# Kernel tuning notes

Measured on AMD Instinct MI355X. Metric: run time of the kernel, lower is better.

The kernel has to match this reference:

```python
import jax, jax.numpy as jnp
import numpy as np

B, C, N = 8, 128, 2048
HEADS = 4
OUT = 128
HD = OUT // HEADS  # 32


def setup_inputs() -> dict:
    key = jax.random.key(0)
    kx, kq, kk, kv, ko = jax.random.split(key, 5)
    # xavier_uniform bounds
    def xavier(k, shape, fan_in, fan_out):
        a = float(np.sqrt(6.0 / (fan_in + fan_out)))
        return jax.random.uniform(k, shape, jnp.float32, -a, a)
    return {
        "x": jax.random.normal(kx, (B, C, N), jnp.float32),
        "W_q": xavier(kq, (HEADS, C, HD), C, HD),
        "W_k": xavier(kk, (HEADS, C, HD), C, HD),
        "W_v": xavier(kv, (HEADS, C, HD), C, HD),
        "W_o": xavier(ko, (OUT, OUT), OUT, OUT),
    }


def reference(x, W_q, W_k, W_v, W_o):
    # x: [B, C, N] -> x_t: [B, N, C]
    x_t = jnp.transpose(x, (0, 2, 1))
    # per-head projections: [B, H, N, d]
    q = jnp.einsum("bnc,hcd->bhnd", x_t, W_q)
    k = jnp.einsum("bnc,hcd->bhnd", x_t, W_k)
    v = jnp.einsum("bnc,hcd->bhnd", x_t, W_v)
    scale = 1.0 / jnp.sqrt(jnp.asarray(HD, jnp.float32))
    # materialized score matrix [B, H, N, N]
    scores = jax.nn.softmax(jnp.einsum("bhnd,bhmd->bhnm", q, k) * scale, axis=-1)
    # weighted sum per head then concat heads: [B, N, H*d]
    out = jnp.einsum("bhnm,bhmd->bhnd", scores, v)
    out = jnp.transpose(out, (0, 2, 1, 3)).reshape(B, N, OUT)
    out = out @ W_o  # [B, N, OUT]
    adj = jnp.mean(scores, axis=1)  # [B, N, N]
    return jnp.transpose(out, (0, 2, 1)), adj
```

## Files before the change

kernel.cpp:

```cpp
#include <hip/hip_runtime.h>
#include <hip/hip_bf16.h>

#define NB 8
#define NC 128
#define NN 2048
#define NH 4
#define HD 32
#define NOUT 128
#define QB 16

typedef _Float16 half8 __attribute__((ext_vector_type(8)));
typedef _Float16 half4 __attribute__((ext_vector_type(4)));
typedef float f32x4 __attribute__((ext_vector_type(4)));

__device__ __forceinline__ f32x4 mfma16(half8 a, half8 b, f32x4 c) {
  return __builtin_amdgcn_mfma_f32_16x16x32_f16(a, b, c, 0, 0, 0);
}

__global__ __launch_bounds__(256) void k_prep(
    const float* __restrict__ Wq, const float* __restrict__ Wk,
    const float* __restrict__ Wv, const float* __restrict__ Wo,
    _Float16* __restrict__ WqT, _Float16* __restrict__ WkT,
    _Float16* __restrict__ WvT, _Float16* __restrict__ WoT)
{
  int id = blockIdx.x * 256 + threadIdx.x;
  if (id < 3 * 16384) {
    int m = id >> 14, rem = id & 16383;
    int h = rem >> 12, d = (rem >> 7) & 31, c = rem & 127;
    const float* W = (m == 0) ? Wq : (m == 1) ? Wk : Wv;
    _Float16* WT   = (m == 0) ? WqT : (m == 1) ? WkT : WvT;
    WT[(h * 32 + d) * 128 + c] = (_Float16)W[(h * 128 + c) * 32 + d];
  } else {
    int j = id - 49152;
    int o = j >> 7, c = j & 127;
    WoT[o * 128 + c] = (_Float16)Wo[c * 128 + o];
  }
}

__global__ __launch_bounds__(256) void k_proj(
    const float* __restrict__ x, const _Float16* __restrict__ WqT,
    const _Float16* __restrict__ WkT, const _Float16* __restrict__ WvT,
    _Float16* __restrict__ qo, _Float16* __restrict__ ko, _Float16* __restrict__ vto)
{
  __shared__ _Float16 xs[32][136];
  const int bid = blockIdx.x;
  const int b  = bid & 7;
  const int n0 = (bid >> 3) * 32;
  const int tid = threadIdx.x;
  const int h = tid >> 6, l = tid & 63, lr = l & 15, lg = l >> 4;

  {
    int c  = tid >> 1;
    int nq = (tid & 1) * 16;
    const float* src = x + (size_t)(b * NC + c) * NN + n0 + nq;
#pragma unroll
    for (int i = 0; i < 4; ++i) {
      f32x4 v = *(const f32x4*)(src + i * 4);
#pragma unroll
      for (int j = 0; j < 4; ++j) xs[nq + i * 4 + j][c] = (_Float16)v[j];
    }
  }
  __syncthreads();

  half8 a[2][4];
#pragma unroll
  for (int rf = 0; rf < 2; ++rf)
#pragma unroll
    for (int kc = 0; kc < 4; ++kc)
      a[rf][kc] = *(const half8*)(&xs[rf * 16 + lr][kc * 32 + lg * 8]);

#pragma unroll
  for (int m = 0; m < 2; ++m) {
    const _Float16* WT = m ? WkT : WqT;
    _Float16* dst      = m ? ko : qo;
    f32x4 acc[2][2] = {};
#pragma unroll
    for (int kc = 0; kc < 4; ++kc) {
      half8 wb[2];
#pragma unroll
      for (int cf = 0; cf < 2; ++cf)
        wb[cf] = *(const half8*)(WT + (size_t)(h * HD + cf * 16 + lr) * NC + kc * 32 + lg * 8);
#pragma unroll
      for (int rf = 0; rf < 2; ++rf)
#pragma unroll
        for (int cf = 0; cf < 2; ++cf)
          acc[rf][cf] = mfma16(a[rf][kc], wb[cf], acc[rf][cf]);
    }
#pragma unroll
    for (int rf = 0; rf < 2; ++rf)
#pragma unroll
      for (int cf = 0; cf < 2; ++cf)
#pragma unroll
        for (int r = 0; r < 4; ++r)
          dst[((size_t)(b * NH + h) * NN + n0 + rf * 16 + lg * 4 + r) * HD + cf * 16 + lr] =
              (_Float16)acc[rf][cf][r];
  }

  {
    f32x4 acc[2][2] = {};
#pragma unroll
    for (int kc = 0; kc < 4; ++kc) {
      half8 aw[2];
#pragma unroll
      for (int rf = 0; rf < 2; ++rf)
        aw[rf] = *(const half8*)(WvT + (size_t)(h * HD + rf * 16 + lr) * NC + kc * 32 + lg * 8);
#pragma unroll
      for (int rf = 0; rf < 2; ++rf)
#pragma unroll
        for (int nf = 0; nf < 2; ++nf)
          acc[rf][nf] = mfma16(aw[rf], a[nf][kc], acc[rf][nf]);
    }
#pragma unroll
    for (int rf = 0; rf < 2; ++rf)
#pragma unroll
      for (int nf = 0; nf < 2; ++nf)
#pragma unroll
        for (int r = 0; r < 4; ++r)
          vto[((size_t)(b * NH + h) * HD + rf * 16 + lg * 4 + r) * NN + n0 + nf * 16 + lr] =
              (_Float16)acc[rf][nf][r];
  }
}

union SMem {
  _Float16 p[NH * QB * 72];
  struct { _Float16 ocat[QB * 136]; float ot[128 * 20]; } ep;
};

__global__ __launch_bounds__(256) void k_attn(
    const _Float16* __restrict__ q, const _Float16* __restrict__ k,
    const _Float16* __restrict__ vt, const _Float16* __restrict__ WoT,
    float* __restrict__ outT, float* __restrict__ adj)
{
  __shared__ SMem sm;
  const int bid = blockIdx.x;
  const int b  = bid & 7;
  const int n0 = (bid >> 3) * QB;
  const int h  = threadIdx.x >> 6;
  const int l  = threadIdx.x & 63;
  const int lr = l & 15, lg = l >> 4;

  const _Float16* qh = q  + (size_t)(b * NH + h) * NN * HD;
  const _Float16* kh = k  + (size_t)(b * NH + h) * NN * HD;
  const _Float16* vh = vt + (size_t)(b * NH + h) * HD * NN;

  half8 qa = *(const half8*)(qh + (size_t)(n0 + lr) * HD + lg * 8);

  const float c1 = 0.25504527f;
  const float c2 = 17.3123405f;

  float rs[4] = {};
  for (int mt = 0; mt < NN / 32; ++mt) {
    half8 kb0 = *(const half8*)(kh + (size_t)(mt * 32 + lr) * HD + lg * 8);
    half8 kb1 = *(const half8*)(kh + (size_t)(mt * 32 + 16 + lr) * HD + lg * 8);
    f32x4 z{};
    f32x4 s0 = mfma16(qa, kb0, z);
    f32x4 s1 = mfma16(qa, kb1, z);
#pragma unroll
    for (int r = 0; r < 4; ++r)
      rs[r] += __builtin_amdgcn_exp2f(s0[r] * c1 - c2) +
               __builtin_amdgcn_exp2f(s1[r] * c1 - c2);
  }
#pragma unroll
  for (int r = 0; r < 4; ++r) {
    float v = rs[r];
    v += __shfl_xor(v, 1); v += __shfl_xor(v, 2);
    v += __shfl_xor(v, 4); v += __shfl_xor(v, 8);
    rs[r] = 1.0f / v;
  }

  f32x4 oacc[2] = {};
  const int tr = threadIdx.x >> 4;
  const int tc = (threadIdx.x & 15) * 4;

  for (int mt2 = 0; mt2 < NN / 64; ++mt2) {
#pragma unroll
    for (int st = 0; st < 4; ++st) {
      half8 kb = *(const half8*)(kh + (size_t)(mt2 * 64 + st * 16 + lr) * HD + lg * 8);
      f32x4 z{};
      f32x4 s = mfma16(qa, kb, z);
#pragma unroll
      for (int r = 0; r < 4; ++r)
        sm.p[(h * QB + lg * 4 + r) * 72 + st * 16 + lr] =
            (_Float16)(__builtin_amdgcn_exp2f(s[r] * c1 - c2) * rs[r]);
    }
    __syncthreads();
#pragma unroll
    for (int kc = 0; kc < 2; ++kc) {
      half8 pa  = *(const half8*)(&sm.p[(h * QB + lr) * 72 + kc * 32 + lg * 8]);
      half8 vb0 = *(const half8*)(vh + (size_t)lr * NN        + mt2 * 64 + kc * 32 + lg * 8);
      half8 vb1 = *(const half8*)(vh + (size_t)(16 + lr) * NN + mt2 * 64 + kc * 32 + lg * 8);
      oacc[0] = mfma16(pa, vb0, oacc[0]);
      oacc[1] = mfma16(pa, vb1, oacc[1]);
    }
    {
      float a4[4] = {};
#pragma unroll
      for (int h2 = 0; h2 < 4; ++h2) {
        half4 pv = *(const half4*)(&sm.p[(h2 * QB + tr) * 72 + tc]);
#pragma unroll
        for (int i = 0; i < 4; ++i) a4[i] += (float)pv[i];
      }
      f32x4 w = {a4[0] * 0.25f, a4[1] * 0.25f, a4[2] * 0.25f, a4[3] * 0.25f};
      *(f32x4*)(adj + ((size_t)(b * NN) + n0 + tr) * NN + mt2 * 64 + tc) = w;
    }
    __syncthreads();
  }

#pragma unroll
  for (int df = 0; df < 2; ++df)
#pragma unroll
    for (int r = 0; r < 4; ++r)
      sm.ep.ocat[(lg * 4 + r) * 136 + h * 32 + df * 16 + lr] = (_Float16)oacc[df][r];
  __syncthreads();

  f32x4 o2[2] = {};
#pragma unroll
  for (int kc = 0; kc < 4; ++kc) {
    half8 a2 = *(const half8*)(&sm.ep.ocat[lr * 136 + kc * 32 + lg * 8]);
#pragma unroll
    for (int of = 0; of < 2; ++of) {
      half8 wb = *(const half8*)(WoT + (size_t)(h * 32 + of * 16 + lr) * NOUT + kc * 32 + lg * 8);
      o2[of] = mfma16(a2, wb, o2[of]);
    }
  }
#pragma unroll
  for (int of = 0; of < 2; ++of)
#pragma unroll
    for (int r = 0; r < 4; ++r)
      sm.ep.ot[(h * 32 + of * 16 + lr) * 20 + lg * 4 + r] = o2[of][r];
  __syncthreads();
  {
    int o  = threadIdx.x >> 1;
    int hf = threadIdx.x & 1;
    float* dst = outT + ((size_t)(b * NOUT) + o) * NN + n0 + hf * 8;
    *(f32x4*)(dst)     = *(const f32x4*)(&sm.ep.ot[o * 20 + hf * 8]);
    *(f32x4*)(dst + 4) = *(const f32x4*)(&sm.ep.ot[o * 20 + hf * 8 + 4]);
  }
}

extern "C" void kernel_launch(void* const* d_in, const int* in_sizes, int n_in,
                              void* d_out, int out_size, void* d_ws, size_t ws_size,
                              hipStream_t stream) {
  const float* x  = (const float*)d_in[0];
  const float* Wq = (const float*)d_in[1];
  const float* Wk = (const float*)d_in[2];
  const float* Wv = (const float*)d_in[3];
  const float* Wo = (const float*)d_in[4];

  float* outT = (float*)d_out;
  float* adj  = outT + (size_t)NB * NOUT * NN;

  const size_t qkv_elems = (size_t)NB * NH * NN * HD;
  _Float16* qw  = (_Float16*)d_ws;
  _Float16* kw  = qw + qkv_elems;
  _Float16* vw  = kw + qkv_elems;
  _Float16* wqT = vw + qkv_elems;
  _Float16* wkT = wqT + 16384;
  _Float16* wvT = wkT + 16384;
  _Float16* woT = wvT + 16384;

  k_prep<<<dim3(256), dim3(256), 0, stream>>>(Wq, Wk, Wv, Wo, wqT, wkT, wvT, woT);
  k_proj<<<dim3(NB * (NN / 32)), dim3(256), 0, stream>>>(x, wqT, wkT, wvT, qw, kw, vw);
  k_attn<<<dim3(NB * (NN / QB)), dim3(256), 0, stream>>>(qw, kw, vw, woT, outT, adj);
}
```

Baseline: 267.1 us.

## Split key dimension across waves with all heads per wave, keep P in registers

```diff
diff --git a/kernel.cpp b/kernel.cpp
--- a/kernel.cpp
+++ b/kernel.cpp
@@ -15,6 +15,9 @@
 
 __device__ __forceinline__ f32x4 mfma16(half8 a, half8 b, f32x4 c) {
   return __builtin_amdgcn_mfma_f32_16x16x32_f16(a, b, c, 0, 0, 0);
+}
+__device__ __forceinline__ f32x4 mfma16k16(half4 a, half4 b, f32x4 c) {
+  return __builtin_amdgcn_mfma_f32_16x16x16f16(a, b, c, 0, 0, 0);
 }
 
 __global__ __launch_bounds__(256) void k_prep(
@@ -121,120 +124,169 @@
   }
 }
 
-union SMem {
-  _Float16 p[NH * QB * 72];
-  struct { _Float16 ocat[QB * 136]; float ot[128 * 20]; } ep;
-};
-
-__global__ __launch_bounds__(256) void k_attn(
+__global__ __launch_bounds__(256, 4) void k_attn(
     const _Float16* __restrict__ q, const _Float16* __restrict__ k,
     const _Float16* __restrict__ vt, const _Float16* __restrict__ WoT,
     float* __restrict__ outT, float* __restrict__ adj)
 {
-  __shared__ SMem sm;
+  __shared__ float r0[4224];
+  __shared__ _Float16 ocat[16 * 136];
+
   const int bid = blockIdx.x;
   const int b  = bid & 7;
   const int n0 = (bid >> 3) * QB;
-  const int h  = threadIdx.x >> 6;
+  const int w  = threadIdx.x >> 6;
   const int l  = threadIdx.x & 63;
   const int lr = l & 15, lg = l >> 4;
 
-  const _Float16* qh = q  + (size_t)(b * NH + h) * NN * HD;
-  const _Float16* kh = k  + (size_t)(b * NH + h) * NN * HD;
-  const _Float16* vh = vt + (size_t)(b * NH + h) * HD * NN;
-
-  half8 qa = *(const half8*)(qh + (size_t)(n0 + lr) * HD + lg * 8);
+  const size_t hstr = (size_t)NN * HD;
+  const _Float16* kb_base = k  + (size_t)b * NH * hstr;
+  const _Float16* vb_base = vt + (size_t)b * NH * hstr;
+  const _Float16* qb_base = q  + (size_t)b * NH * hstr;
+
+  half8 qa[NH];
+#pragma unroll
+  for (int h = 0; h < NH; ++h)
+    qa[h] = *(const half8*)(qb_base + h * hstr + (size_t)(n0 + lr) * HD + lg * 8);
 
   const float c1 = 0.25504527f;
   const float c2 = 17.3123405f;
-
-  float rs[4] = {};
-  for (int mt = 0; mt < NN / 32; ++mt) {
-    half8 kb0 = *(const half8*)(kh + (size_t)(mt * 32 + lr) * HD + lg * 8);
-    half8 kb1 = *(const half8*)(kh + (size_t)(mt * 32 + 16 + lr) * HD + lg * 8);
-    f32x4 z{};
-    f32x4 s0 = mfma16(qa, kb0, z);
-    f32x4 s1 = mfma16(qa, kb1, z);
+  const f32x4 z{};
+
+  float rs[NH] = {};
+  {
+    const _Float16* kp = kb_base + (size_t)(w * 16 + lr) * HD + lg * 8;
+    for (int t = 0; t < NN / 64; ++t) {
+      half8 kb[NH];
+#pragma unroll
+      for (int h = 0; h < NH; ++h) kb[h] = *(const half8*)(kp + h * hstr);
+      f32x4 s[NH];
+#pragma unroll
+      for (int h = 0; h < NH; ++h) s[h] = mfma16(kb[h], qa[h], z);
+#pragma unroll
+      for (int h = 0; h < NH; ++h)
+        rs[h] += (__builtin_amdgcn_exp2f(s[h][0] * c1 - c2) +
+                  __builtin_amdgcn_exp2f(s[h][1] * c1 - c2)) +
+                 (__builtin_amdgcn_exp2f(s[h][2] * c1 - c2) +
+                  __builtin_amdgcn_exp2f(s[h][3] * c1 - c2));
+      kp += 64 * HD;
+    }
+  }
+#pragma unroll
+  for (int h = 0; h < NH; ++h) {
+    rs[h] += __shfl_xor(rs[h], 16);
+    rs[h] += __shfl_xor(rs[h], 32);
+  }
+  {
+    float v = (lg == 0) ? rs[0] : (lg == 1) ? rs[1] : (lg == 2) ? rs[2] : rs[3];
+    r0[w * 64 + lg * 16 + lr] = v;
+  }
+  __syncthreads();
+  float ah[NH];
+#pragma unroll
+  for (int h = 0; h < NH; ++h) {
+    float S = r0[h * 16 + lr] + r0[64 + h * 16 + lr] +
+              r0[128 + h * 16 + lr] + r0[192 + h * 16 + lr];
+    ah[h] = -c2 - __builtin_amdgcn_logf(S);
+  }
+  __syncthreads();
+
+  f32x4 oacc[NH][2] = {};
+  {
+    const _Float16* kp  = kb_base + (size_t)(w * 16 + lr) * HD + lg * 8;
+    const _Float16* vp0 = vb_base + (size_t)lr * NN + w * 16 + lg * 4;
+    const _Float16* vp1 = vb_base + (size_t)(16 + lr) * NN + w * 16 + lg * 4;
+    float* adjp = adj + ((size_t)b * NN + n0 + lr) * NN + w * 16 + lg * 4;
+    for (int t = 0; t < NN / 64; ++t) {
+      half8 kb[NH];
+#pragma unroll
+      for (int h = 0; h < NH; ++h) kb[h] = *(const half8*)(kp + h * hstr);
+      f32x4 s[NH];
+#pragma unroll
+      for (int h = 0; h < NH; ++h) s[h] = mfma16(kb[h], qa[h], z);
+      half4 vb0[NH], vb1[NH];
+#pragma unroll
+      for (int h = 0; h < NH; ++h) {
+        vb0[h] = *(const half4*)(vp0 + h * hstr);
+        vb1[h] = *(const half4*)(vp1 + h * hstr);
+      }
+      f32x4 adjv{};
+      half4 pa[NH];
+#pragma unroll
+      for (int h = 0; h < NH; ++h) {
+        float p0 = __builtin_amdgcn_exp2f(s[h][0] * c1 + ah[h]);
+        float p1 = __builtin_amdgcn_exp2f(s[h][1] * c1 + ah[h]);
+        float p2 = __builtin_amdgcn_exp2f(s[h][2] * c1 + ah[h]);
+        float p3 = __builtin_amdgcn_exp2f(s[h][3] * c1 + ah[h]);
+        adjv[0] += p0; adjv[1] += p1; adjv[2] += p2; adjv[3] += p3;
+        pa[h] = half4{(_Float16)p0, (_Float16)p1, (_Float16)p2, (_Float16)p3};
+      }
+#pragma unroll
+      for (int h = 0; h < NH; ++h) {
+        oacc[h][0] = mfma16k16(pa[h], vb0[h], oacc[h][0]);
+        oacc[h][1] = mfma16k16(pa[h], vb1[h], oacc[h][1]);
+      }
+      f32x4 av = adjv * 0.25f;
+      *(f32x4*)adjp = av;
+      kp += 64 * HD; vp0 += 64; vp1 += 64; adjp += 64;
+    }
+  }
+
+  {
+    float* buf = &r0[(w & 1) * 2112];
+    if (w < 2) {
+#pragma unroll
+      for (int h = 0; h < NH; ++h)
+#pragma unroll
+        for (int df = 0; df < 2; ++df)
+#pragma unroll
+          for (int r = 0; r < 4; ++r)
+            buf[(lg * 4 + r) * 132 + h * 32 + df * 16 + lr] = oacc[h][df][r];
+    }
+    __syncthreads();
+    if (w >= 2) {
+#pragma unroll
+      for (int h = 0; h < NH; ++h)
+#pragma unroll
+        for (int df = 0; df < 2; ++df)
+#pragma unroll
+          for (int r = 0; r < 4; ++r)
+            buf[(lg * 4 + r) * 132 + h * 32 + df * 16 + lr] += oacc[h][df][r];
+    }
+    __syncthreads();
+  }
+  {
+    int n = threadIdx.x >> 4, d8 = (threadIdx.x & 15) * 8;
+    half8 hv;
+#pragma unroll
+    for (int j = 0; j < 8; ++j)
+      hv[j] = (_Float16)(r0[n * 132 + d8 + j] + r0[2112 + n * 132 + d8 + j]);
+    *(half8*)&ocat[n * 136 + d8] = hv;
+  }
+  __syncthreads();
+
+  f32x4 o2[2] = {};
+#pragma unroll
+  for (int kc = 0; kc < 4; ++kc) {
+    half8 a2 = *(const half8*)&ocat[lr * 136 + kc * 32 + lg * 8];
+#pragma unroll
+    for (int of = 0; of < 2; ++of) {
+      half8 wb = *(const half8*)(WoT + (size_t)(w * 32 + of * 16 + lr) * NOUT + kc * 32 + lg * 8);
+      o2[of] = mfma16(a2, wb, o2[of]);
+    }
+  }
+#pragma unroll
+  for (int of = 0; of < 2; ++of)
 #pragma unroll
     for (int r = 0; r < 4; ++r)
-      rs[r] += __builtin_amdgcn_exp2f(s0[r] * c1 - c2) +
-               __builtin_amdgcn_exp2f(s1[r] * c1 - c2);
-  }
-#pragma unroll
-  for (int r = 0; r < 4; ++r) {
-    float v = rs[r];
-    v += __shfl_xor(v, 1); v += __shfl_xor(v, 2);
-    v += __shfl_xor(v, 4); v += __shfl_xor(v, 8);
-    rs[r] = 1.0f / v;
-  }
-
-  f32x4 oacc[2] = {};
-  const int tr = threadIdx.x >> 4;
-  const int tc = (threadIdx.x & 15) * 4;
-
-  for (int mt2 = 0; mt2 < NN / 64; ++mt2) {
-#pragma unroll
-    for (int st = 0; st < 4; ++st) {
-      half8 kb = *(const half8*)(kh + (size_t)(mt2 * 64 + st * 16 + lr) * HD + lg * 8);
-      f32x4 z{};
-      f32x4 s = mfma16(qa, kb, z);
-#pragma unroll
-      for (int r = 0; r < 4; ++r)
-        sm.p[(h * QB + lg * 4 + r) * 72 + st * 16 + lr] =
-            (_Float16)(__builtin_amdgcn_exp2f(s[r] * c1 - c2) * rs[r]);
-    }
-    __syncthreads();
-#pragma unroll
-    for (int kc = 0; kc < 2; ++kc) {
-      half8 pa  = *(const half8*)(&sm.p[(h * QB + lr) * 72 + kc * 32 + lg * 8]);
-      half8 vb0 = *(const half8*)(vh + (size_t)lr * NN        + mt2 * 64 + kc * 32 + lg * 8);
-      half8 vb1 = *(const half8*)(vh + (size_t)(16 + lr) * NN + mt2 * 64 + kc * 32 + lg * 8);
-      oacc[0] = mfma16(pa, vb0, oacc[0]);
-      oacc[1] = mfma16(pa, vb1, oacc[1]);
-    }
-    {
-      float a4[4] = {};
-#pragma unroll
-      for (int h2 = 0; h2 < 4; ++h2) {
-        half4 pv = *(const half4*)(&sm.p[(h2 * QB + tr) * 72 + tc]);
-#pragma unroll
-        for (int i = 0; i < 4; ++i) a4[i] += (float)pv[i];
-      }
-      f32x4 w = {a4[0] * 0.25f, a4[1] * 0.25f, a4[2] * 0.25f, a4[3] * 0.25f};
-      *(f32x4*)(adj + ((size_t)(b * NN) + n0 + tr) * NN + mt2 * 64 + tc) = w;
-    }
-    __syncthreads();
-  }
-
-#pragma unroll
-  for (int df = 0; df < 2; ++df)
-#pragma unroll
-    for (int r = 0; r < 4; ++r)
-      sm.ep.ocat[(lg * 4 + r) * 136 + h * 32 + df * 16 + lr] = (_Float16)oacc[df][r];
-  __syncthreads();
-
-  f32x4 o2[2] = {};
-#pragma unroll
-  for (int kc = 0; kc < 4; ++kc) {
-    half8 a2 = *(const half8*)(&sm.ep.ocat[lr * 136 + kc * 32 + lg * 8]);
-#pragma unroll
-    for (int of = 0; of < 2; ++of) {
-      half8 wb = *(const half8*)(WoT + (size_t)(h * 32 + of * 16 + lr) * NOUT + kc * 32 + lg * 8);
-      o2[of] = mfma16(a2, wb, o2[of]);
-    }
-  }
-#pragma unroll
-  for (int of = 0; of < 2; ++of)
-#pragma unroll
-    for (int r = 0; r < 4; ++r)
-      sm.ep.ot[(h * 32 + of * 16 + lr) * 20 + lg * 4 + r] = o2[of][r];
+      r0[(w * 32 + of * 16 + lr) * 20 + lg * 4 + r] = o2[of][r];
   __syncthreads();
   {
     int o  = threadIdx.x >> 1;
     int hf = threadIdx.x & 1;
     float* dst = outT + ((size_t)(b * NOUT) + o) * NN + n0 + hf * 8;
-    *(f32x4*)(dst)     = *(const f32x4*)(&sm.ep.ot[o * 20 + hf * 8]);
-    *(f32x4*)(dst + 4) = *(const f32x4*)(&sm.ep.ot[o * 20 + hf * 8 + 4]);
+    *(f32x4*)dst       = *(const f32x4*)&r0[o * 20 + hf * 8];
+    *(f32x4*)(dst + 4) = *(const f32x4*)&r0[o * 20 + hf * 8 + 4];
   }
 }
 
```

After: 321.7 us. 1.2x slower.
